# Performance work log

Hardware: AMD Instinct MI355X
Metric: run time of the kernel (lower is better)

The kernel has to match this reference:

```python
import jax, jax.numpy as jnp
import numpy as np

NEG_INF = -1e16


def setup_inputs() -> dict:
    key = jax.random.key(0)
    k1, k2, k3 = jax.random.split(key, 3)
    B, N, C, D = 8, 4096, 64, 64
    inputs = jax.random.normal(k1, (B, N, C), dtype=jnp.float32)
    graph = jax.random.randint(k2, (N, N), 0, 2, dtype=jnp.int32)
    # xavier_uniform for Linear weight [D, C]
    limit = float(np.sqrt(6.0 / (C + D)))
    W = jax.random.uniform(k3, (D, C), dtype=jnp.float32, minval=-limit, maxval=limit)
    b = jnp.zeros((D,), dtype=jnp.float32)
    return {"inputs": inputs, "graph": graph, "W": W, "b": b}


def reference(inputs, graph, W, b):
    # h = W(inputs): [B, N, D]
    h = jnp.einsum('bnc,dc->bnd', inputs, W)
    # dense pairwise scores: [B, N, N]
    scores = jnp.einsum('bnd,bmd->bnm', h, h)
    # mask non-edges (graph broadcasts over batch)
    scores = jnp.where(graph[None, :, :] == 0, NEG_INF, scores)
    attention = jax.nn.softmax(scores, axis=2)
    out = jnp.einsum('bnm,bmd->bnd', attention, h) + b
    return out
```

## Files before the change

### kernel.cpp

```cpp
#include <hip/hip_runtime.h>
#include <stdint.h>

typedef _Float16 f16x8 __attribute__((ext_vector_type(8)));
typedef _Float16 f16x4 __attribute__((ext_vector_type(4)));
typedef __fp16 half2_t __attribute__((ext_vector_type(2)));
typedef float f32x4 __attribute__((ext_vector_type(4)));

#define LOG2E 1.44269504088896340736f
#define NEGINF (-1e16f)

constexpr int kN = 4096;
constexpr int kD = 64;
constexpr int kB = 8;

__global__ __launch_bounds__(256) void hproj_kernel(const float* __restrict__ x,
                                                    const float* __restrict__ W,
                                                    _Float16* __restrict__ hout,
                                                    _Float16* __restrict__ hTout)
{
    __shared__ float Wt[64][64];
    __shared__ float xs[64][65];
    __shared__ _Float16 ht[64][68];

    const int tid = threadIdx.x;
    const int r   = tid >> 2;
    const int c0  = (tid & 3) * 16;

    #pragma unroll
    for (int j = 0; j < 16; j += 4) {
        const float4 v = *(const float4*)(W + r * 64 + c0 + j);
        Wt[c0 + j + 0][r] = v.x;
        Wt[c0 + j + 1][r] = v.y;
        Wt[c0 + j + 2][r] = v.z;
        Wt[c0 + j + 3][r] = v.w;
    }
    const long rowbase = (long)blockIdx.x * 64;
    #pragma unroll
    for (int j = 0; j < 16; j += 4) {
        const float4 v = *(const float4*)(x + (rowbase + r) * 64 + c0 + j);
        xs[r][c0 + j + 0] = v.x;
        xs[r][c0 + j + 1] = v.y;
        xs[r][c0 + j + 2] = v.z;
        xs[r][c0 + j + 3] = v.w;
    }
    __syncthreads();

    const int d0 = (tid & 3) * 16;
    f32x4 acc[4] = {{0.f,0.f,0.f,0.f},{0.f,0.f,0.f,0.f},{0.f,0.f,0.f,0.f},{0.f,0.f,0.f,0.f}};
    #pragma unroll 4
    for (int c = 0; c < 64; ++c) {
        const float xv = xs[r][c];
        const f32x4* wrow = (const f32x4*)&Wt[c][d0];
        #pragma unroll
        for (int k = 0; k < 4; ++k) acc[k] += wrow[k] * xv;
    }
    f16x8 o0, o1;
    #pragma unroll
    for (int j = 0; j < 8; ++j) {
        o0[j] = (_Float16)acc[j >> 2][j & 3];
        o1[j] = (_Float16)acc[2 + (j >> 2)][j & 3];
    }
    *(f16x8*)(hout + (rowbase + r) * 64 + d0)     = o0;
    *(f16x8*)(hout + (rowbase + r) * 64 + d0 + 8) = o1;

    #pragma unroll
    for (int j = 0; j < 8; ++j) {
        ht[r][d0 + j]     = o0[j];
        ht[r][d0 + 8 + j] = o1[j];
    }
    __syncthreads();

    const int bb = blockIdx.x >> 6;
    const int n0 = (int)(rowbase & (kN - 1));
    const int dr = tid >> 2;
    const int c4 = (tid & 3) * 16;
    f16x8 t0, t1;
    #pragma unroll
    for (int j = 0; j < 8; ++j) {
        t0[j] = ht[c4 + j][dr];
        t1[j] = ht[c4 + 8 + j][dr];
    }
    _Float16* dst = hTout + (long)bb * kD * kN + (long)dr * kN + n0 + c4;
    *(f16x8*)(dst)     = t0;
    *(f16x8*)(dst + 8) = t1;
}

__global__ __launch_bounds__(256) void bitpack_kernel(const int* __restrict__ g,
                                                      uint32_t* __restrict__ mw)
{
    const long w = (long)blockIdx.x * 256 + threadIdx.x;
    const int4* p = (const int4*)(g + w * 32);
    uint32_t bits = 0;
    #pragma unroll
    for (int j = 0; j < 8; ++j) {
        const int4 v = p[j];
        bits |= (uint32_t)(v.x != 0) << (j * 4 + 0);
        bits |= (uint32_t)(v.y != 0) << (j * 4 + 1);
        bits |= (uint32_t)(v.z != 0) << (j * 4 + 2);
        bits |= (uint32_t)(v.w != 0) << (j * 4 + 3);
    }
    mw[w] = bits;
}

__global__ __launch_bounds__(256) void masktr_kernel(const uint32_t* __restrict__ mw,
                                                     uint64_t* __restrict__ wmout)
{
    const int tid  = threadIdx.x;
    const int wv   = tid >> 6;
    const int lane = tid & 63;
    const int ll   = lane & 15;
    const int lg   = lane >> 4;
    const int pair = blockIdx.x * 4 + wv;
    const int q16  = pair >> 6;
    const int kv64 = pair & 63;

    const uint2 u = *(const uint2*)(mw + (long)(q16 * 16 + ll) * 128 + kv64 * 2);

    uint64_t Wb[16];
    #pragma unroll
    for (int s = 0; s < 16; ++s) {
        const int t = s >> 2, rr = s & 3;
        const uint32_t word = (t >= 2) ? u.y : u.x;
        const int pos = 8 * lg + 4 * (t & 1) + rr;
        Wb[s] = __ballot(((word >> pos) & 1u) != 0);
    }

    const int s = lane;
    uint64_t a0 = (s & 1) ? Wb[1]  : Wb[0];
    uint64_t a1 = (s & 1) ? Wb[3]  : Wb[2];
    uint64_t a2 = (s & 1) ? Wb[5]  : Wb[4];
    uint64_t a3 = (s & 1) ? Wb[7]  : Wb[6];
    uint64_t a4 = (s & 1) ? Wb[9]  : Wb[8];
    uint64_t a5 = (s & 1) ? Wb[11] : Wb[10];
    uint64_t a6 = (s & 1) ? Wb[13] : Wb[12];
    uint64_t a7 = (s & 1) ? Wb[15] : Wb[14];
    uint64_t b0 = (s & 2) ? a1 : a0;
    uint64_t b1 = (s & 2) ? a3 : a2;
    uint64_t b2 = (s & 2) ? a5 : a4;
    uint64_t b3 = (s & 2) ? a7 : a6;
    uint64_t c0 = (s & 4) ? b1 : b0;
    uint64_t c1 = (s & 4) ? b3 : b2;
    uint64_t v  = (s & 8) ? c1 : c0;
    if (lane < 16) wmout[(long)pair * 16 + lane] = v;
}

__global__ __launch_bounds__(512) void attn_kernel(const _Float16* __restrict__ h,
                                                   const _Float16* __restrict__ hT,
                                                   const uint64_t* __restrict__ wmask,
                                                   const float* __restrict__ bias,
                                                   float* __restrict__ outp,
                                                   _Float16* __restrict__ pO,
                                                   float* __restrict__ pml,
                                                   int kvlen)
{
    __shared__ alignas(16) char Kl[2][8192];
    __shared__ alignas(16) char Vt[2][8192];

    const int b     = blockIdx.y;
    const int split = blockIdx.z;
    const int q0    = blockIdx.x * 128;
    const int tid   = threadIdx.x;
    const int wave  = tid >> 6;
    const int lane  = tid & 63;
    const int lg    = lane >> 4;
    const int ll    = lane & 15;

    const _Float16* hb  = h  + (long)b * kN * kD;
    const _Float16* hTb = hT + (long)b * kD * kN;
    const int kv_base = split * kvlen;
    const int NT      = kvlen / 64;

    const int q = q0 + wave * 16 + ll;
    const f16x8 qf0 = *(const f16x8*)(hb + q * 64 + lg * 8);
    const f16x8 qf1 = *(const f16x8*)(hb + q * 64 + 32 + lg * 8);

    f16x8 vone;
    {
        const _Float16 o = (ll == 0) ? (_Float16)1.0f : (_Float16)0.0f;
        #pragma unroll
        for (int j = 0; j < 8; ++j) vone[j] = o;
    }

    f32x4 Oacc[4] = {{0.f,0.f,0.f,0.f},{0.f,0.f,0.f,0.f},{0.f,0.f,0.f,0.f},{0.f,0.f,0.f,0.f}};
    f32x4 Oacc4 = {0.f, 0.f, 0.f, 0.f};
    float m_run = NEGINF;
    float mm = NEGINF * LOG2E;
    float negv = NEGINF;

    const int sr  = tid >> 3;
    const int sc8 = (tid & 7) * 8;
    const int srp = (sr & 0x23) | ((sr & 0x18) >> 1) | ((sr & 0x4) << 2);

    const int kw = srp * 128 + ((sc8 * 2) ^ ((srp & 7) << 4));
    const int vw = sr  * 128 + ((sc8 * 2) ^ ((sr  & 7) << 4));
    const int rb0 = ll * 128 + (((lg * 16))      ^ ((ll & 7) << 4));
    const int rb1 = ll * 128 + (((64 + lg * 16)) ^ ((ll & 7) << 4));

    char* const KB = (char*)Kl;
    char* const VB = (char*)Vt;

    const _Float16* gK = hb  + (long)(kv_base + sr) * 64 + sc8;
    const _Float16* gV = hTb + (long)sr * kN + kv_base + sc8;

    const int wuni = __builtin_amdgcn_readfirstlane(wave);
    const uint64_t* __restrict__ wmp =
        wmask + ((long)(blockIdx.x * 8 + wuni) * 64 + (kv_base >> 6)) * 16;

    uint64_t wmA[16], wmB[16];
    {
        const f16x8 a0 = *(const f16x8*)(gK);
        const f16x8 b0 = *(const f16x8*)(gV);
        *(f16x8*)(KB + kw) = a0;
        *(f16x8*)(VB + vw) = b0;
        gK += 64 * 64;  gV += 64;
        #pragma unroll
        for (int s = 0; s < 16; ++s) wmA[s] = wmp[s];
    }

#define TILE_BODY(WMC, WMN, IT, CB, NB)                                          \
    do {                                                                         \
        const int it_ = (IT);                                                    \
                  \
        f16x8 nk0{}, nv0{};                                                      \
        if (it_ + 1 < NT) {                                                      \
            nk0 = *(const f16x8*)(gK);                                           \
            nv0 = *(const f16x8*)(gV);                                           \
            gK += 64 * 64;  gV += 64;                                            \
        }                                                                        \
                    \
        asm volatile("s_waitcnt lgkmcnt(0)" ::: "memory");                       \
        __builtin_amdgcn_s_barrier();                                            \
        __builtin_amdgcn_sched_barrier(0);                                       \
                       \
        if (it_ + 1 < NT) {                                                      \
            _Pragma("unroll")                                                    \
            for (int s5 = 0; s5 < 16; ++s5) WMN[s5] = wmp[(long)(it_+1)*16 + s5];\
        }                                                                        \
        f32x4 S[4];                                                              \
        _Pragma("unroll")                                                        \
        for (int t = 0; t < 4; ++t) {                                            \
            const f16x8 k0 = *(const f16x8*)(KB + (CB) + rb0 + t * 2048);        \
            const f16x8 k1 = *(const f16x8*)(KB + (CB) + rb1 + t * 2048);        \
            f32x4 s = {0.f, 0.f, 0.f, 0.f};                                      \
            s = __builtin_amdgcn_mfma_f32_16x16x32_f16(k0, qf0, s, 0, 0, 0);     \
            s = __builtin_amdgcn_mfma_f32_16x16x32_f16(k1, qf1, s, 0, 0, 0);     \
            S[t] = s;                                                            \
        }                                                                        \
            \
        if (it_ + 1 < NT) {                                                      \
            *(f16x8*)(KB + (NB) + kw) = nk0;                                     \
            *(f16x8*)(VB + (NB) + vw) = nv0;                                     \
        }                                                                        \
        _Pragma("unroll")                                                        \
        for (int t = 0; t < 4; ++t) {                                            \
            _Pragma("unroll")                                                    \
            for (int rr = 0; rr < 4; ++rr) {                                     \
                float sv = S[t][rr];                                             \
                asm("v_cndmask_b32 %0, %1, %2, %3"                               \
                    : "=v"(sv) : "v"(negv), "v"(sv), "s"(WMC[t * 4 + rr]));      \
                S[t][rr] = sv;                                                   \
            }                                                                    \
        }                                                                        \
                                \
        float mx0 = fmaxf(fmaxf(fmaxf(S[0][0], S[0][1]), S[0][2]), S[0][3]);     \
        float mx1 = fmaxf(fmaxf(fmaxf(S[1][0], S[1][1]), S[1][2]), S[1][3]);     \
        float mx2 = fmaxf(fmaxf(fmaxf(S[2][0], S[2][1]), S[2][2]), S[2][3]);     \
        float mx3 = fmaxf(fmaxf(fmaxf(S[3][0], S[3][1]), S[3][2]), S[3][3]);     \
        float mloc = fmaxf(fmaxf(fmaxf(mx0, mx1), mx2), mx3);                    \
        mloc = fmaxf(mloc, __shfl_xor(mloc, 16));                                \
        mloc = fmaxf(mloc, __shfl_xor(mloc, 32));                                \
        if (__any(mloc > m_run + 8.f)) {                                         \
            const float mnew = fmaxf(m_run, mloc);                               \
            const float scl  = __builtin_amdgcn_exp2f((m_run - mnew) * LOG2E);   \
            m_run = mnew;                                                        \
            mm    = mnew * LOG2E;                                                \
            _Pragma("unroll")                                                    \
            for (int dt = 0; dt < 4; ++dt) Oacc[dt] *= scl;                      \
            Oacc4 *= scl;                                                        \
        }                                                                        \
        _Pragma("unroll")                                                        \
        for (int t = 0; t < 4; ++t) {                                            \
            _Pragma("unroll")                                                    \
            for (int rr = 0; rr < 4; ++rr)                                       \
                S[t][rr] = __builtin_amdgcn_exp2f(fmaf(S[t][rr], LOG2E, -mm));   \
        }                                                                        \
        union PF { half2_t hh[4]; f16x8 v; };                                    \
        PF pf1, pf2;                                                             \
        pf1.hh[0] = __builtin_amdgcn_cvt_pkrtz(S[0][0], S[0][1]);                \
        pf1.hh[1] = __builtin_amdgcn_cvt_pkrtz(S[0][2], S[0][3]);                \
        pf1.hh[2] = __builtin_amdgcn_cvt_pkrtz(S[1][0], S[1][1]);                \
        pf1.hh[3] = __builtin_amdgcn_cvt_pkrtz(S[1][2], S[1][3]);                \
        pf2.hh[0] = __builtin_amdgcn_cvt_pkrtz(S[2][0], S[2][1]);                \
        pf2.hh[1] = __builtin_amdgcn_cvt_pkrtz(S[2][2], S[2][3]);                \
        pf2.hh[2] = __builtin_amdgcn_cvt_pkrtz(S[3][0], S[3][1]);                \
        pf2.hh[3] = __builtin_amdgcn_cvt_pkrtz(S[3][2], S[3][3]);                \
        _Pragma("unroll")                                                        \
        for (int dt = 0; dt < 4; ++dt) {                                         \
            const f16x8 v0 = *(const f16x8*)(VB + (CB) + rb0 + dt * 2048);       \
            const f16x8 v1 = *(const f16x8*)(VB + (CB) + rb1 + dt * 2048);       \
            Oacc[dt] = __builtin_amdgcn_mfma_f32_16x16x32_f16(v0, pf1.v, Oacc[dt], 0, 0, 0); \
            Oacc[dt] = __builtin_amdgcn_mfma_f32_16x16x32_f16(v1, pf2.v, Oacc[dt], 0, 0, 0); \
        }                                                                        \
        Oacc4 = __builtin_amdgcn_mfma_f32_16x16x32_f16(vone, pf1.v, Oacc4, 0, 0, 0); \
        Oacc4 = __builtin_amdgcn_mfma_f32_16x16x32_f16(vone, pf2.v, Oacc4, 0, 0, 0); \
    } while (0)

    for (int ith = 0; ith < NT; ith += 2) {
        TILE_BODY(wmA, wmB, ith,     0,    8192);
        TILE_BODY(wmB, wmA, ith + 1, 8192, 0);
    }
#undef TILE_BODY

    const float lsum = __shfl(Oacc4[0], ll, 64);
    const float inv  = (lsum > 0.f) ? (1.0f / lsum) : 0.f;

    if (outp != nullptr) {
        #pragma unroll
        for (int dt = 0; dt < 4; ++dt) {
            const int dbase = dt * 16 + lg * 4;
            const f32x4 bv = *(const f32x4*)(bias + dbase);
            f32x4 o;
            #pragma unroll
            for (int rr = 0; rr < 4; ++rr) o[rr] = Oacc[dt][rr] * inv + bv[rr];
            *(f32x4*)(outp + ((long)b * kN + q) * 64 + dbase) = o;
        }
    } else {
        const long srow = (long)split * kB * kN + (long)b * kN + q;
        #pragma unroll
        for (int dt = 0; dt < 4; ++dt) {
            const int dbase = dt * 16 + lg * 4;
            f16x4 po;
            #pragma unroll
            for (int rr = 0; rr < 4; ++rr) po[rr] = (_Float16)(Oacc[dt][rr] * inv);
            *(f16x4*)(pO + srow * 64 + dbase) = po;
        }
        if (lane < 16) {
            pml[srow * 2 + 0] = m_run;
            pml[srow * 2 + 1] = lsum;
        }
    }
}

__global__ __launch_bounds__(256) void combine_kernel(const _Float16* __restrict__ pO,
                                                      const float* __restrict__ pml,
                                                      const float* __restrict__ bias,
                                                      float* __restrict__ outp,
                                                      int ks)
{
    const long idx = (long)blockIdx.x * 256 + threadIdx.x;
    const long row = idx >> 4;
    const int  d4  = (int)(idx & 15) * 4;

    float M = NEGINF;
    for (int s = 0; s < ks; ++s)
        M = fmaxf(M, pml[((long)s * kB * kN + row) * 2]);

    float L = 0.f;
    f32x4 acc = {0.f, 0.f, 0.f, 0.f};
    for (int s = 0; s < ks; ++s) {
        const long srow = (long)s * kB * kN + row;
        const float m = pml[srow * 2 + 0];
        const float l = pml[srow * 2 + 1];
        const float w = l * __builtin_amdgcn_exp2f((m - M) * LOG2E);
        L += w;
        const f16x4 o = *(const f16x4*)(pO + srow * 64 + d4);
        #pragma unroll
        for (int j = 0; j < 4; ++j) acc[j] += (float)o[j] * w;
    }
    const float invL = (L > 0.f) ? (1.0f / L) : 0.f;
    const f32x4 bv = *(const f32x4*)(bias + d4);
    *(f32x4*)(outp + row * 64 + d4) = acc * invL + bv;
}

extern "C" void kernel_launch(void* const* d_in, const int* in_sizes, int n_in,
                              void* d_out, int out_size, void* d_ws, size_t ws_size,
                              hipStream_t stream) {
    const float*  x     = (const float*)d_in[0];
    const int*    graph = (const int*)d_in[1];
    const float*  W     = (const float*)d_in[2];
    const float*  bias  = (const float*)d_in[3];
    float*        outp  = (float*)d_out;

    char* ws = (char*)d_ws;
    _Float16* hptr  = (_Float16*)ws;
    uint32_t* mwptr = (uint32_t*)(ws + (4u << 20));
    _Float16* hTptr = (_Float16*)(ws + (6u << 20));
    uint64_t* wmptr = (uint64_t*)(ws + (10u << 20));

    int ks = 1;
    if      (ws_size >= ((size_t)47 << 20)) ks = 8;
    else if (ws_size >= ((size_t)30 << 20)) ks = 4;
    else if (ws_size >= ((size_t)21 << 20)) ks = 2;

    _Float16* pO  = (_Float16*)(ws + (12u << 20));
    float*    pml = (float*)(ws + (12u << 20) + (size_t)ks * (4u << 20));

    hproj_kernel<<<dim3(kB * kN / 64), dim3(256), 0, stream>>>(x, W, hptr, hTptr);
    bitpack_kernel<<<dim3(kN * (kN / 32) / 256), dim3(256), 0, stream>>>(graph, mwptr);
    masktr_kernel<<<dim3(256 * 64 / 4), dim3(256), 0, stream>>>(mwptr, wmptr);

    if (ks == 1) {
        attn_kernel<<<dim3(kN / 128, kB, 1), dim3(512), 0, stream>>>(
            hptr, hTptr, wmptr, bias, outp, nullptr, nullptr, kN);
    } else {
        attn_kernel<<<dim3(kN / 128, kB, ks), dim3(512), 0, stream>>>(
            hptr, hTptr, wmptr, bias, nullptr, pO, pml, kN / ks);
        combine_kernel<<<dim3(kB * kN * 16 / 256), dim3(256), 0, stream>>>(
            pO, pml, bias, outp, ks);
    }
}
```

Before: 93.78 us.

## Process two KV tiles per iteration with 128-wide blocks and cap split-K at 4

The attention loop now handles 128 keys per iteration, with double-buffered pairs of 64-key tiles in LDS (64KB total). This halves the number of barriers and online-softmax rescale checks per key and gives longer MFMA chains. The mask words are now loaded after the barrier inside each iteration instead of being prefetched one tile ahead. The maximum KV split drops from 8 to 4, so each block does more work and there is less combine traffic, at the cost of fewer blocks and lower occupancy from the larger LDS use.

```diff
diff --git a/kernel.cpp b/kernel.cpp
--- a/kernel.cpp
+++ b/kernel.cpp
@@ -153,8 +153,8 @@
                                                    float* __restrict__ pml,
                                                    int kvlen)
 {
-    __shared__ alignas(16) char Kl[2][8192];
-    __shared__ alignas(16) char Vt[2][8192];
+    __shared__ alignas(16) char Kl[4][8192];
+    __shared__ alignas(16) char Vt[4][8192];
 
     const int b     = blockIdx.y;
     const int split = blockIdx.z;
@@ -168,7 +168,7 @@
     const _Float16* hb  = h  + (long)b * kN * kD;
     const _Float16* hTb = hT + (long)b * kD * kN;
     const int kv_base = split * kvlen;
-    const int NT      = kvlen / 64;
+    const int NP      = kvlen / 128;
 
     const int q = q0 + wave * 16 + ll;
     const f16x8 qf0 = *(const f16x8*)(hb + q * 64 + lg * 8);
@@ -206,67 +206,76 @@
     const uint64_t* __restrict__ wmp =
         wmask + ((long)(blockIdx.x * 8 + wuni) * 64 + (kv_base >> 6)) * 16;
 
-    uint64_t wmA[16], wmB[16];
     {
         const f16x8 a0 = *(const f16x8*)(gK);
+        const f16x8 a1 = *(const f16x8*)(gK + 4096);
         const f16x8 b0 = *(const f16x8*)(gV);
-        *(f16x8*)(KB + kw) = a0;
-        *(f16x8*)(VB + vw) = b0;
-        gK += 64 * 64;  gV += 64;
-        #pragma unroll
-        for (int s = 0; s < 16; ++s) wmA[s] = wmp[s];
-    }
-
-#define TILE_BODY(WMC, WMN, IT, CB, NB)                                          \
+        const f16x8 b1 = *(const f16x8*)(gV + 64);
+        *(f16x8*)(KB + kw)        = a0;
+        *(f16x8*)(KB + 8192 + kw) = a1;
+        *(f16x8*)(VB + vw)        = b0;
+        *(f16x8*)(VB + 8192 + vw) = b1;
+        gK += 8192;  gV += 128;
+    }
+
+#define PAIR_BODY(IP, CB, NB)                                                    \
     do {                                                                         \
-        const int it_ = (IT);                                                    \
+        const int ip_ = (IP);                                                    \
                   \
-        f16x8 nk0{}, nv0{};                                                      \
-        if (it_ + 1 < NT) {                                                      \
+        f16x8 nk0{}, nk1{}, nv0{}, nv1{};                                        \
+        if (ip_ + 1 < NP) {                                                      \
             nk0 = *(const f16x8*)(gK);                                           \
+            nk1 = *(const f16x8*)(gK + 4096);                                    \
             nv0 = *(const f16x8*)(gV);                                           \
-            gK += 64 * 64;  gV += 64;                                            \
-        }                                                                        \
-                    \
+            nv1 = *(const f16x8*)(gV + 64);                                      \
+            gK += 8192;  gV += 128;                                              \
+        }                                                                        \
+                         \
         asm volatile("s_waitcnt lgkmcnt(0)" ::: "memory");                       \
         __builtin_amdgcn_s_barrier();                                            \
         __builtin_amdgcn_sched_barrier(0);                                       \
-                       \
-        if (it_ + 1 < NT) {                                                      \
-            _Pragma("unroll")                                                    \
-            for (int s5 = 0; s5 < 16; ++s5) WMN[s5] = wmp[(long)(it_+1)*16 + s5];\
-        }                                                                        \
-        f32x4 S[4];                                                              \
-        _Pragma("unroll")                                                        \
-        for (int t = 0; t < 4; ++t) {                                            \
-            const f16x8 k0 = *(const f16x8*)(KB + (CB) + rb0 + t * 2048);        \
-            const f16x8 k1 = *(const f16x8*)(KB + (CB) + rb1 + t * 2048);        \
+             \
+        uint64_t WM[32];                                                         \
+        _Pragma("unroll")                                                        \
+        for (int s5 = 0; s5 < 32; ++s5) WM[s5] = wmp[(long)ip_ * 32 + s5];       \
+                               \
+        f32x4 S[8];                                                              \
+        _Pragma("unroll")                                                        \
+        for (int t2 = 0; t2 < 8; ++t2) {                                         \
+            const int kbase = (CB) + (t2 >> 2) * 8192 + (t2 & 3) * 2048;         \
+            const f16x8 k0 = *(const f16x8*)(KB + kbase + rb0);                  \
+            const f16x8 k1 = *(const f16x8*)(KB + kbase + rb1);                  \
             f32x4 s = {0.f, 0.f, 0.f, 0.f};                                      \
             s = __builtin_amdgcn_mfma_f32_16x16x32_f16(k0, qf0, s, 0, 0, 0);     \
             s = __builtin_amdgcn_mfma_f32_16x16x32_f16(k1, qf1, s, 0, 0, 0);     \
-            S[t] = s;                                                            \
-        }                                                                        \
-            \
-        if (it_ + 1 < NT) {                                                      \
-            *(f16x8*)(KB + (NB) + kw) = nk0;                                     \
-            *(f16x8*)(VB + (NB) + vw) = nv0;                                     \
-        }                                                                        \
-        _Pragma("unroll")                                                        \
-        for (int t = 0; t < 4; ++t) {                                            \
+            S[t2] = s;                                                           \
+        }                                                                        \
+                             \
+        if (ip_ + 1 < NP) {                                                      \
+            *(f16x8*)(KB + (NB) + kw)        = nk0;                              \
+            *(f16x8*)(KB + (NB) + 8192 + kw) = nk1;                              \
+            *(f16x8*)(VB + (NB) + vw)        = nv0;                              \
+            *(f16x8*)(VB + (NB) + 8192 + vw) = nv1;                              \
+        }                                                                        \
+                 \
+        _Pragma("unroll")                                                        \
+        for (int t2 = 0; t2 < 8; ++t2) {                                         \
             _Pragma("unroll")                                                    \
             for (int rr = 0; rr < 4; ++rr) {                                     \
-                float sv = S[t][rr];                                             \
+                float sv = S[t2][rr];                                            \
                 asm("v_cndmask_b32 %0, %1, %2, %3"                               \
-                    : "=v"(sv) : "v"(negv), "v"(sv), "s"(WMC[t * 4 + rr]));      \
-                S[t][rr] = sv;                                                   \
+                    : "=v"(sv)                                                   \
+                    : "v"(negv), "v"(sv),                                        \
+                      "s"(WM[(t2 >> 2) * 16 + (t2 & 3) * 4 + rr]));              \
+                S[t2][rr] = sv;                                                  \
             }                                                                    \
         }                                                                        \
-                                \
-        float mx0 = fmaxf(fmaxf(fmaxf(S[0][0], S[0][1]), S[0][2]), S[0][3]);     \
-        float mx1 = fmaxf(fmaxf(fmaxf(S[1][0], S[1][1]), S[1][2]), S[1][3]);     \
-        float mx2 = fmaxf(fmaxf(fmaxf(S[2][0], S[2][1]), S[2][2]), S[2][3]);     \
-        float mx3 = fmaxf(fmaxf(fmaxf(S[3][0], S[3][1]), S[3][2]), S[3][3]);     \
-        float mloc = fmaxf(fmaxf(fmaxf(mx0, mx1), mx2), mx3);                    \
+                                                \
+        float mloc = NEGINF;                                                     \
+        _Pragma("unroll")                                                        \
+        for (int t2 = 0; t2 < 8; ++t2)                                           \
+            mloc = fmaxf(mloc,                                                   \
+                   fmaxf(fmaxf(S[t2][0], S[t2][1]), fmaxf(S[t2][2], S[t2][3]))); \
         mloc = fmaxf(mloc, __shfl_xor(mloc, 16));                                \
         mloc = fmaxf(mloc, __shfl_xor(mloc, 32));                                \
         if (__any(mloc > m_run + 8.f)) {                                         \
@@ -279,37 +288,45 @@
             Oacc4 *= scl;                                                        \
         }                                                                        \
         _Pragma("unroll")                                                        \
-        for (int t = 0; t < 4; ++t) {                                            \
+        for (int t2 = 0; t2 < 8; ++t2) {                                         \
             _Pragma("unroll")                                                    \
             for (int rr = 0; rr < 4; ++rr)                                       \
-                S[t][rr] = __builtin_amdgcn_exp2f(fmaf(S[t][rr], LOG2E, -mm));   \
+                S[t2][rr] = __builtin_amdgcn_exp2f(fmaf(S[t2][rr], LOG2E, -mm)); \
         }                                                                        \
         union PF { half2_t hh[4]; f16x8 v; };                                    \
-        PF pf1, pf2;                                                             \
-        pf1.hh[0] = __builtin_amdgcn_cvt_pkrtz(S[0][0], S[0][1]);                \
-        pf1.hh[1] = __builtin_amdgcn_cvt_pkrtz(S[0][2], S[0][3]);                \
-        pf1.hh[2] = __builtin_amdgcn_cvt_pkrtz(S[1][0], S[1][1]);                \
-        pf1.hh[3] = __builtin_amdgcn_cvt_pkrtz(S[1][2], S[1][3]);                \
-        pf2.hh[0] = __builtin_amdgcn_cvt_pkrtz(S[2][0], S[2][1]);                \
-        pf2.hh[1] = __builtin_amdgcn_cvt_pkrtz(S[2][2], S[2][3]);                \
-        pf2.hh[2] = __builtin_amdgcn_cvt_pkrtz(S[3][0], S[3][1]);                \
-        pf2.hh[3] = __builtin_amdgcn_cvt_pkrtz(S[3][2], S[3][3]);                \
+        PF pf[4];                                                                \
+        _Pragma("unroll")                                                        \
+        for (int pp = 0; pp < 4; ++pp) {                                         \
+            pf[pp].hh[0] = __builtin_amdgcn_cvt_pkrtz(S[pp*2][0],   S[pp*2][1]); \
+            pf[pp].hh[1] = __builtin_amdgcn_cvt_pkrtz(S[pp*2][2],   S[pp*2][3]); \
+            pf[pp].hh[2] = __builtin_amdgcn_cvt_pkrtz(S[pp*2+1][0], S[pp*2+1][1]);\
+            pf[pp].hh[3] = __builtin_amdgcn_cvt_pkrtz(S[pp*2+1][2], S[pp*2+1][3]);\
+        }                                                                        \
+                                            \
         _Pragma("unroll")                                                        \
         for (int dt = 0; dt < 4; ++dt) {                                         \
-            const f16x8 v0 = *(const f16x8*)(VB + (CB) + rb0 + dt * 2048);       \
-            const f16x8 v1 = *(const f16x8*)(VB + (CB) + rb1 + dt * 2048);       \
-            Oacc[dt] = __builtin_amdgcn_mfma_f32_16x16x32_f16(v0, pf1.v, Oacc[dt], 0, 0, 0); \
-            Oacc[dt] = __builtin_amdgcn_mfma_f32_16x16x32_f16(v1, pf2.v, Oacc[dt], 0, 0, 0); \
-        }                                                                        \
-        Oacc4 = __builtin_amdgcn_mfma_f32_16x16x32_f16(vone, pf1.v, Oacc4, 0, 0, 0); \
-        Oacc4 = __builtin_amdgcn_mfma_f32_16x16x32_f16(vone, pf2.v, Oacc4, 0, 0, 0); \
+            const int vb0 = (CB) + rb0 + dt * 2048;                              \
+            const int vb1 = (CB) + rb1 + dt * 2048;                              \
+            const f16x8 v0 = *(const f16x8*)(VB + vb0);                          \
+            const f16x8 v1 = *(const f16x8*)(VB + vb1);                          \
+            const f16x8 v2 = *(const f16x8*)(VB + vb0 + 8192);                   \
+            const f16x8 v3 = *(const f16x8*)(VB + vb1 + 8192);                   \
+            Oacc[dt] = __builtin_amdgcn_mfma_f32_16x16x32_f16(v0, pf[0].v, Oacc[dt], 0, 0, 0); \
+            Oacc[dt] = __builtin_amdgcn_mfma_f32_16x16x32_f16(v1, pf[1].v, Oacc[dt], 0, 0, 0); \
+            Oacc[dt] = __builtin_amdgcn_mfma_f32_16x16x32_f16(v2, pf[2].v, Oacc[dt], 0, 0, 0); \
+            Oacc[dt] = __builtin_amdgcn_mfma_f32_16x16x32_f16(v3, pf[3].v, Oacc[dt], 0, 0, 0); \
+        }                                                                        \
+        Oacc4 = __builtin_amdgcn_mfma_f32_16x16x32_f16(vone, pf[0].v, Oacc4, 0, 0, 0); \
+        Oacc4 = __builtin_amdgcn_mfma_f32_16x16x32_f16(vone, pf[1].v, Oacc4, 0, 0, 0); \
+        Oacc4 = __builtin_amdgcn_mfma_f32_16x16x32_f16(vone, pf[2].v, Oacc4, 0, 0, 0); \
+        Oacc4 = __builtin_amdgcn_mfma_f32_16x16x32_f16(vone, pf[3].v, Oacc4, 0, 0, 0); \
     } while (0)
 
-    for (int ith = 0; ith < NT; ith += 2) {
-        TILE_BODY(wmA, wmB, ith,     0,    8192);
-        TILE_BODY(wmB, wmA, ith + 1, 8192, 0);
-    }
-#undef TILE_BODY
+    for (int ipp = 0; ipp < NP; ipp += 2) {
+        PAIR_BODY(ipp,     0,     16384);
+        PAIR_BODY(ipp + 1, 16384, 0);
+    }
+#undef PAIR_BODY
 
     const float lsum = __shfl(Oacc4[0], ll, 64);
     const float inv  = (lsum > 0.f) ? (1.0f / lsum) : 0.f;
@@ -388,8 +405,7 @@
     uint64_t* wmptr = (uint64_t*)(ws + (10u << 20));
 
     int ks = 1;
-    if      (ws_size >= ((size_t)47 << 20)) ks = 8;
-    else if (ws_size >= ((size_t)30 << 20)) ks = 4;
+    if      (ws_size >= ((size_t)30 << 20)) ks = 4;
     else if (ws_size >= ((size_t)21 << 20)) ks = 2;
 
     _Float16* pO  = (_Float16*)(ws + (12u << 20));
```

After: 87.24 us. -7.0%, faster.

## Process two 16-query fragments per wave to reuse K/V tiles

Applied to the files above, without the earlier changes.

Each wave now handles 32 query rows instead of 16, so every K and V fragment loaded from LDS feeds two MFMA chains. This halves the LDS traffic and barrier count per query. The block covers 256 queries, the split-K factor is capped at 4, MFMA sections are wrapped in s_setprio, and mask words are loaded in the same tile rather than prefetched a tile ahead. The price is doubled accumulator register pressure under launch_bounds(512,4), fewer blocks in the grid, and exposed mask-load latency.

```diff
diff --git a/kernel.cpp b/kernel.cpp
--- a/kernel.cpp
+++ b/kernel.cpp
@@ -144,21 +144,21 @@
     if (lane < 16) wmout[(long)pair * 16 + lane] = v;
 }
 
-__global__ __launch_bounds__(512) void attn_kernel(const _Float16* __restrict__ h,
-                                                   const _Float16* __restrict__ hT,
-                                                   const uint64_t* __restrict__ wmask,
-                                                   const float* __restrict__ bias,
-                                                   float* __restrict__ outp,
-                                                   _Float16* __restrict__ pO,
-                                                   float* __restrict__ pml,
-                                                   int kvlen)
+__global__ __launch_bounds__(512, 4) void attn_kernel(const _Float16* __restrict__ h,
+                                                      const _Float16* __restrict__ hT,
+                                                      const uint64_t* __restrict__ wmask,
+                                                      const float* __restrict__ bias,
+                                                      float* __restrict__ outp,
+                                                      _Float16* __restrict__ pO,
+                                                      float* __restrict__ pml,
+                                                      int kvlen)
 {
     __shared__ alignas(16) char Kl[2][8192];
     __shared__ alignas(16) char Vt[2][8192];
 
     const int b     = blockIdx.y;
     const int split = blockIdx.z;
-    const int q0    = blockIdx.x * 128;
+    const int q0    = blockIdx.x * 256;
     const int tid   = threadIdx.x;
     const int wave  = tid >> 6;
     const int lane  = tid & 63;
@@ -170,9 +170,12 @@
     const int kv_base = split * kvlen;
     const int NT      = kvlen / 64;
 
-    const int q = q0 + wave * 16 + ll;
-    const f16x8 qf0 = *(const f16x8*)(hb + q * 64 + lg * 8);
-    const f16x8 qf1 = *(const f16x8*)(hb + q * 64 + 32 + lg * 8);
+    const int qA = q0 + wave * 32 + ll;
+    const int qB = qA + 16;
+    const f16x8 qfA0 = *(const f16x8*)(hb + qA * 64 + lg * 8);
+    const f16x8 qfA1 = *(const f16x8*)(hb + qA * 64 + 32 + lg * 8);
+    const f16x8 qfB0 = *(const f16x8*)(hb + qB * 64 + lg * 8);
+    const f16x8 qfB1 = *(const f16x8*)(hb + qB * 64 + 32 + lg * 8);
 
     f16x8 vone;
     {
@@ -181,10 +184,12 @@
         for (int j = 0; j < 8; ++j) vone[j] = o;
     }
 
-    f32x4 Oacc[4] = {{0.f,0.f,0.f,0.f},{0.f,0.f,0.f,0.f},{0.f,0.f,0.f,0.f},{0.f,0.f,0.f,0.f}};
-    f32x4 Oacc4 = {0.f, 0.f, 0.f, 0.f};
-    float m_run = NEGINF;
-    float mm = NEGINF * LOG2E;
+    f32x4 OaccA[4] = {{0.f,0.f,0.f,0.f},{0.f,0.f,0.f,0.f},{0.f,0.f,0.f,0.f},{0.f,0.f,0.f,0.f}};
+    f32x4 OaccB[4] = {{0.f,0.f,0.f,0.f},{0.f,0.f,0.f,0.f},{0.f,0.f,0.f,0.f},{0.f,0.f,0.f,0.f}};
+    f32x4 Oacc4A = {0.f, 0.f, 0.f, 0.f};
+    f32x4 Oacc4B = {0.f, 0.f, 0.f, 0.f};
+    float m_runA = NEGINF, m_runB = NEGINF;
+    float mmA = NEGINF * LOG2E, mmB = NEGINF * LOG2E;
     float negv = NEGINF;
 
     const int sr  = tid >> 3;
@@ -203,21 +208,65 @@
     const _Float16* gV = hTb + (long)sr * kN + kv_base + sc8;
 
     const int wuni = __builtin_amdgcn_readfirstlane(wave);
-    const uint64_t* __restrict__ wmp =
-        wmask + ((long)(blockIdx.x * 8 + wuni) * 64 + (kv_base >> 6)) * 16;
-
-    uint64_t wmA[16], wmB[16];
+    const uint64_t* __restrict__ wmpA =
+        wmask + ((long)(blockIdx.x * 16 + wuni * 2) * 64 + (kv_base >> 6)) * 16;
+    const uint64_t* __restrict__ wmpB = wmpA + (long)64 * 16;
+
     {
         const f16x8 a0 = *(const f16x8*)(gK);
         const f16x8 b0 = *(const f16x8*)(gV);
         *(f16x8*)(KB + kw) = a0;
         *(f16x8*)(VB + vw) = b0;
         gK += 64 * 64;  gV += 64;
-        #pragma unroll
-        for (int s = 0; s < 16; ++s) wmA[s] = wmp[s];
-    }
-
-#define TILE_BODY(WMC, WMN, IT, CB, NB)                                          \
+    }
+
+    union PF { half2_t hh[4]; f16x8 v; };
+
+#define SOFTMAX_FRAG(S_, WM_, OACC_, OACC4_, MRUN_, MM_, PF1_, PF2_)             \
+    do {                                                                         \
+        _Pragma("unroll")                                                        \
+        for (int t = 0; t < 4; ++t) {                                            \
+            _Pragma("unroll")                                                    \
+            for (int rr = 0; rr < 4; ++rr) {                                     \
+                float sv = S_[t][rr];                                            \
+                asm("v_cndmask_b32 %0, %1, %2, %3"                               \
+                    : "=v"(sv) : "v"(negv), "v"(sv), "s"(WM_[t * 4 + rr]));      \
+                S_[t][rr] = sv;                                                  \
+            }                                                                    \
+        }                                                                        \
+        float mx0 = fmaxf(fmaxf(S_[0][0], S_[0][1]), fmaxf(S_[0][2], S_[0][3])); \
+        float mx1 = fmaxf(fmaxf(S_[1][0], S_[1][1]), fmaxf(S_[1][2], S_[1][3])); \
+        float mx2 = fmaxf(fmaxf(S_[2][0], S_[2][1]), fmaxf(S_[2][2], S_[2][3])); \
+        float mx3 = fmaxf(fmaxf(S_[3][0], S_[3][1]), fmaxf(S_[3][2], S_[3][3])); \
+        float mloc = fmaxf(fmaxf(mx0, mx1), fmaxf(mx2, mx3));                    \
+        mloc = fmaxf(mloc, __shfl_xor(mloc, 16));                                \
+        mloc = fmaxf(mloc, __shfl_xor(mloc, 32));                                \
+        if (__any(mloc > MRUN_ + 8.f)) {                                         \
+            const float mnew = fmaxf(MRUN_, mloc);                               \
+            const float scl  = __builtin_amdgcn_exp2f((MRUN_ - mnew) * LOG2E);   \
+            MRUN_ = mnew;                                                        \
+            MM_   = mnew * LOG2E;                                                \
+            _Pragma("unroll")                                                    \
+            for (int dt = 0; dt < 4; ++dt) OACC_[dt] *= scl;                     \
+            OACC4_ *= scl;                                                       \
+        }                                                                        \
+        _Pragma("unroll")                                                        \
+        for (int t = 0; t < 4; ++t) {                                            \
+            _Pragma("unroll")                                                    \
+            for (int rr = 0; rr < 4; ++rr)                                       \
+                S_[t][rr] = __builtin_amdgcn_exp2f(fmaf(S_[t][rr], LOG2E, -MM_));\
+        }                                                                        \
+        PF1_.hh[0] = __builtin_amdgcn_cvt_pkrtz(S_[0][0], S_[0][1]);             \
+        PF1_.hh[1] = __builtin_amdgcn_cvt_pkrtz(S_[0][2], S_[0][3]);             \
+        PF1_.hh[2] = __builtin_amdgcn_cvt_pkrtz(S_[1][0], S_[1][1]);             \
+        PF1_.hh[3] = __builtin_amdgcn_cvt_pkrtz(S_[1][2], S_[1][3]);             \
+        PF2_.hh[0] = __builtin_amdgcn_cvt_pkrtz(S_[2][0], S_[2][1]);             \
+        PF2_.hh[1] = __builtin_amdgcn_cvt_pkrtz(S_[2][2], S_[2][3]);             \
+        PF2_.hh[2] = __builtin_amdgcn_cvt_pkrtz(S_[3][0], S_[3][1]);             \
+        PF2_.hh[3] = __builtin_amdgcn_cvt_pkrtz(S_[3][2], S_[3][3]);             \
+    } while (0)
+
+#define TILE_BODY(IT, CB, NB)                                                    \
     do {                                                                         \
         const int it_ = (IT);                                                    \
                   \
@@ -227,116 +276,105 @@
             nv0 = *(const f16x8*)(gV);                                           \
             gK += 64 * 64;  gV += 64;                                            \
         }                                                                        \
-                    \
+                         \
         asm volatile("s_waitcnt lgkmcnt(0)" ::: "memory");                       \
         __builtin_amdgcn_s_barrier();                                            \
         __builtin_amdgcn_sched_barrier(0);                                       \
-                       \
-        if (it_ + 1 < NT) {                                                      \
-            _Pragma("unroll")                                                    \
-            for (int s5 = 0; s5 < 16; ++s5) WMN[s5] = wmp[(long)(it_+1)*16 + s5];\
-        }                                                                        \
-        f32x4 S[4];                                                              \
+                \
+        uint64_t WMA[16], WMB[16];                                               \
+        _Pragma("unroll")                                                        \
+        for (int s5 = 0; s5 < 16; ++s5) WMA[s5] = wmpA[(long)it_ * 16 + s5];     \
+        _Pragma("unroll")                                                        \
+        for (int s5 = 0; s5 < 16; ++s5) WMB[s5] = wmpB[(long)it_ * 16 + s5];     \
+                                       \
+        f32x4 SA[4], SB[4];                                                      \
+        __builtin_amdgcn_s_setprio(1);                                           \
         _Pragma("unroll")                                                        \
         for (int t = 0; t < 4; ++t) {                                            \
             const f16x8 k0 = *(const f16x8*)(KB + (CB) + rb0 + t * 2048);        \
             const f16x8 k1 = *(const f16x8*)(KB + (CB) + rb1 + t * 2048);        \
-            f32x4 s = {0.f, 0.f, 0.f, 0.f};                                      \
-            s = __builtin_amdgcn_mfma_f32_16x16x32_f16(k0, qf0, s, 0, 0, 0);     \
-            s = __builtin_amdgcn_mfma_f32_16x16x32_f16(k1, qf1, s, 0, 0, 0);     \
-            S[t] = s;                                                            \
-        }                                                                        \
-            \
+            f32x4 sa = {0.f, 0.f, 0.f, 0.f};                                     \
+            f32x4 sb = {0.f, 0.f, 0.f, 0.f};                                     \
+            sa = __builtin_amdgcn_mfma_f32_16x16x32_f16(k0, qfA0, sa, 0, 0, 0);  \
+            sa = __builtin_amdgcn_mfma_f32_16x16x32_f16(k1, qfA1, sa, 0, 0, 0);  \
+            sb = __builtin_amdgcn_mfma_f32_16x16x32_f16(k0, qfB0, sb, 0, 0, 0);  \
+            sb = __builtin_amdgcn_mfma_f32_16x16x32_f16(k1, qfB1, sb, 0, 0, 0);  \
+            SA[t] = sa;                                                          \
+            SB[t] = sb;                                                          \
+        }                                                                        \
+        __builtin_amdgcn_s_setprio(0);                                           \
+                                  \
         if (it_ + 1 < NT) {                                                      \
             *(f16x8*)(KB + (NB) + kw) = nk0;                                     \
             *(f16x8*)(VB + (NB) + vw) = nv0;                                     \
         }                                                                        \
-        _Pragma("unroll")                                                        \
-        for (int t = 0; t < 4; ++t) {                                            \
-            _Pragma("unroll")                                                    \
-            for (int rr = 0; rr < 4; ++rr) {                                     \
-                float sv = S[t][rr];                                             \
-                asm("v_cndmask_b32 %0, %1, %2, %3"                               \
-                    : "=v"(sv) : "v"(negv), "v"(sv), "s"(WMC[t * 4 + rr]));      \
-                S[t][rr] = sv;                                                   \
-            }                                                                    \
-        }                                                                        \
-                                \
-        float mx0 = fmaxf(fmaxf(fmaxf(S[0][0], S[0][1]), S[0][2]), S[0][3]);     \
-        float mx1 = fmaxf(fmaxf(fmaxf(S[1][0], S[1][1]), S[1][2]), S[1][3]);     \
-        float mx2 = fmaxf(fmaxf(fmaxf(S[2][0], S[2][1]), S[2][2]), S[2][3]);     \
-        float mx3 = fmaxf(fmaxf(fmaxf(S[3][0], S[3][1]), S[3][2]), S[3][3]);     \
-        float mloc = fmaxf(fmaxf(fmaxf(mx0, mx1), mx2), mx3);                    \
-        mloc = fmaxf(mloc, __shfl_xor(mloc, 16));                                \
-        mloc = fmaxf(mloc, __shfl_xor(mloc, 32));                                \
-        if (__any(mloc > m_run + 8.f)) {                                         \
-            const float mnew = fmaxf(m_run, mloc);                               \
-            const float scl  = __builtin_amdgcn_exp2f((m_run - mnew) * LOG2E);   \
-            m_run = mnew;                                                        \
-            mm    = mnew * LOG2E;                                                \
-            _Pragma("unroll")                                                    \
-            for (int dt = 0; dt < 4; ++dt) Oacc[dt] *= scl;                      \
-            Oacc4 *= scl;                                                        \
-        }                                                                        \
-        _Pragma("unroll")                                                        \
-        for (int t = 0; t < 4; ++t) {                                            \
-            _Pragma("unroll")                                                    \
-            for (int rr = 0; rr < 4; ++rr)                                       \
-                S[t][rr] = __builtin_amdgcn_exp2f(fmaf(S[t][rr], LOG2E, -mm));   \
-        }                                                                        \
-        union PF { half2_t hh[4]; f16x8 v; };                                    \
-        PF pf1, pf2;                                                             \
-        pf1.hh[0] = __builtin_amdgcn_cvt_pkrtz(S[0][0], S[0][1]);                \
-        pf1.hh[1] = __builtin_amdgcn_cvt_pkrtz(S[0][2], S[0][3]);                \
-        pf1.hh[2] = __builtin_amdgcn_cvt_pkrtz(S[1][0], S[1][1]);                \
-        pf1.hh[3] = __builtin_amdgcn_cvt_pkrtz(S[1][2], S[1][3]);                \
-        pf2.hh[0] = __builtin_amdgcn_cvt_pkrtz(S[2][0], S[2][1]);                \
-        pf2.hh[1] = __builtin_amdgcn_cvt_pkrtz(S[2][2], S[2][3]);                \
-        pf2.hh[2] = __builtin_amdgcn_cvt_pkrtz(S[3][0], S[3][1]);                \
-        pf2.hh[3] = __builtin_amdgcn_cvt_pkrtz(S[3][2], S[3][3]);                \
+        PF pfA1, pfA2, pfB1, pfB2;                                               \
+        SOFTMAX_FRAG(SA, WMA, OaccA, Oacc4A, m_runA, mmA, pfA1, pfA2);           \
+        SOFTMAX_FRAG(SB, WMB, OaccB, Oacc4B, m_runB, mmB, pfB1, pfB2);           \
+                                       \
+        __builtin_amdgcn_s_setprio(1);                                           \
         _Pragma("unroll")                                                        \
         for (int dt = 0; dt < 4; ++dt) {                                         \
             const f16x8 v0 = *(const f16x8*)(VB + (CB) + rb0 + dt * 2048);       \
             const f16x8 v1 = *(const f16x8*)(VB + (CB) + rb1 + dt * 2048);       \
-            Oacc[dt] = __builtin_amdgcn_mfma_f32_16x16x32_f16(v0, pf1.v, Oacc[dt], 0, 0, 0); \
-            Oacc[dt] = __builtin_amdgcn_mfma_f32_16x16x32_f16(v1, pf2.v, Oacc[dt], 0, 0, 0); \
-        }                                                                        \
-        Oacc4 = __builtin_amdgcn_mfma_f32_16x16x32_f16(vone, pf1.v, Oacc4, 0, 0, 0); \
-        Oacc4 = __builtin_amdgcn_mfma_f32_16x16x32_f16(vone, pf2.v, Oacc4, 0, 0, 0); \
+            OaccA[dt] = __builtin_amdgcn_mfma_f32_16x16x32_f16(v0, pfA1.v, OaccA[dt], 0, 0, 0); \
+            OaccA[dt] = __builtin_amdgcn_mfma_f32_16x16x32_f16(v1, pfA2.v, OaccA[dt], 0, 0, 0); \
+            OaccB[dt] = __builtin_amdgcn_mfma_f32_16x16x32_f16(v0, pfB1.v, OaccB[dt], 0, 0, 0); \
+            OaccB[dt] = __builtin_amdgcn_mfma_f32_16x16x32_f16(v1, pfB2.v, OaccB[dt], 0, 0, 0); \
+        }                                                                        \
+        Oacc4A = __builtin_amdgcn_mfma_f32_16x16x32_f16(vone, pfA1.v, Oacc4A, 0, 0, 0); \
+        Oacc4A = __builtin_amdgcn_mfma_f32_16x16x32_f16(vone, pfA2.v, Oacc4A, 0, 0, 0); \
+        Oacc4B = __builtin_amdgcn_mfma_f32_16x16x32_f16(vone, pfB1.v, Oacc4B, 0, 0, 0); \
+        Oacc4B = __builtin_amdgcn_mfma_f32_16x16x32_f16(vone, pfB2.v, Oacc4B, 0, 0, 0); \
+        __builtin_amdgcn_s_setprio(0);                                           \
     } while (0)
 
     for (int ith = 0; ith < NT; ith += 2) {
-        TILE_BODY(wmA, wmB, ith,     0,    8192);
-        TILE_BODY(wmB, wmA, ith + 1, 8192, 0);
+        TILE_BODY(ith,     0,    8192);
+        TILE_BODY(ith + 1, 8192, 0);
     }
 #undef TILE_BODY
-
-    const float lsum = __shfl(Oacc4[0], ll, 64);
-    const float inv  = (lsum > 0.f) ? (1.0f / lsum) : 0.f;
+#undef SOFTMAX_FRAG
+
+    const float lsumA = __shfl(Oacc4A[0], ll, 64);
+    const float lsumB = __shfl(Oacc4B[0], ll, 64);
+    const float invA  = (lsumA > 0.f) ? (1.0f / lsumA) : 0.f;
+    const float invB  = (lsumB > 0.f) ? (1.0f / lsumB) : 0.f;
 
     if (outp != nullptr) {
         #pragma unroll
         for (int dt = 0; dt < 4; ++dt) {
             const int dbase = dt * 16 + lg * 4;
             const f32x4 bv = *(const f32x4*)(bias + dbase);
-            f32x4 o;
+            f32x4 oa, ob;
             #pragma unroll
-            for (int rr = 0; rr < 4; ++rr) o[rr] = Oacc[dt][rr] * inv + bv[rr];
-            *(f32x4*)(outp + ((long)b * kN + q) * 64 + dbase) = o;
+            for (int rr = 0; rr < 4; ++rr) {
+                oa[rr] = OaccA[dt][rr] * invA + bv[rr];
+                ob[rr] = OaccB[dt][rr] * invB + bv[rr];
+            }
+            *(f32x4*)(outp + ((long)b * kN + qA) * 64 + dbase) = oa;
+            *(f32x4*)(outp + ((long)b * kN + qB) * 64 + dbase) = ob;
         }
     } else {
-        const long srow = (long)split * kB * kN + (long)b * kN + q;
+        const long srowA = (long)split * kB * kN + (long)b * kN + qA;
+        const long srowB = srowA + 16;
         #pragma unroll
         for (int dt = 0; dt < 4; ++dt) {
             const int dbase = dt * 16 + lg * 4;
-            f16x4 po;
+            f16x4 pa, pb;
             #pragma unroll
-            for (int rr = 0; rr < 4; ++rr) po[rr] = (_Float16)(Oacc[dt][rr] * inv);
-            *(f16x4*)(pO + srow * 64 + dbase) = po;
+            for (int rr = 0; rr < 4; ++rr) {
+                pa[rr] = (_Float16)(OaccA[dt][rr] * invA);
+                pb[rr] = (_Float16)(OaccB[dt][rr] * invB);
+            }
+            *(f16x4*)(pO + srowA * 64 + dbase) = pa;
+            *(f16x4*)(pO + srowB * 64 + dbase) = pb;
         }
         if (lane < 16) {
-            pml[srow * 2 + 0] = m_run;
-            pml[srow * 2 + 1] = lsum;
+            pml[srowA * 2 + 0] = m_runA;
+            pml[srowA * 2 + 1] = lsumA;
+            pml[srowB * 2 + 0] = m_runB;
+            pml[srowB * 2 + 1] = lsumB;
         }
     }
 }
@@ -388,8 +426,7 @@
     uint64_t* wmptr = (uint64_t*)(ws + (10u << 20));
 
     int ks = 1;
-    if      (ws_size >= ((size_t)47 << 20)) ks = 8;
-    else if (ws_size >= ((size_t)30 << 20)) ks = 4;
+    if      (ws_size >= ((size_t)30 << 20)) ks = 4;
     else if (ws_size >= ((size_t)21 << 20)) ks = 2;
 
     _Float16* pO  = (_Float16*)(ws + (12u << 20));
@@ -400,10 +437,10 @@
     masktr_kernel<<<dim3(256 * 64 / 4), dim3(256), 0, stream>>>(mwptr, wmptr);
 
     if (ks == 1) {
-        attn_kernel<<<dim3(kN / 128, kB, 1), dim3(512), 0, stream>>>(
+        attn_kernel<<<dim3(kN / 256, kB, 1), dim3(512), 0, stream>>>(
             hptr, hTptr, wmptr, bias, outp, nullptr, nullptr, kN);
     } else {
-        attn_kernel<<<dim3(kN / 128, kB, ks), dim3(512), 0, stream>>>(
+        attn_kernel<<<dim3(kN / 256, kB, ks), dim3(512), 0, stream>>>(
             hptr, hTptr, wmptr, bias, nullptr, pO, pml, kN / ks);
         combine_kernel<<<dim3(kB * kN * 16 / 256), dim3(256), 0, stream>>>(
             pO, pml, bias, outp, ks);
```

Measured after the change: 85.23 us. 9.1% less time.
